# Optimization experiments

Hardware: AMD Instinct MI355X
Metric: run time of the kernel (lower is better)

The kernel has to match this reference:

```python
import jax, jax.numpy as jnp
import numpy as np

B, D, O = 1024, 512, 256


def setup_inputs() -> dict:
    key = jax.random.key(0)
    kx, kw, kt = jax.random.split(key, 3)
    x = jax.random.uniform(kx, (B, D), dtype=jnp.float32)
    w = jax.random.uniform(kw, (D, O), dtype=jnp.float32)
    t = jax.random.uniform(kt, (B, O), dtype=jnp.float32)
    return {"x": x, "w": w, "t": t}


def reference(x, w, t):
    xe = x[:, :, None]   # [B, D, 1]
    te = t[:, None, :]   # [B, 1, O]
    we = w[None, :, :]   # [1, D, O]

    x_comp = 1.0 - xe    # [B, D, 1]
    t_comp = 1.0 - te    # [B, 1, O]
    w_comp = 1.0 - we    # [1, D, O]

    # rel_x: [1, D, O]; sum over batch dim 0 of broadcasted min
    rel_x = 1.0 - (jnp.sum(jnp.minimum(x_comp, t_comp), axis=0, keepdims=True)
                   / jnp.sum(x_comp, axis=0, keepdims=True))
    # rel_w: [B, 1, O]; sum over D dim of broadcasted min
    rel_w = 1.0 - (jnp.sum(jnp.minimum(w_comp, t_comp), axis=-2, keepdims=True)
                   / jnp.sum(w_comp, axis=-2, keepdims=True))

    ind_x = jnp.argmin(jnp.maximum(xe, rel_x), axis=-2, keepdims=True)  # [B, 1, O]
    ind_w = jnp.argmin(jnp.maximum(rel_w, we), axis=-2, keepdims=True)  # [B, 1, O]

    inner_x = jnp.maximum(xe, jax.lax.stop_gradient(we))  # [B, D, O]
    inner_w = jnp.maximum(jax.lax.stop_gradient(xe), we)  # [B, D, O]

    chosen_x = jnp.take_along_axis(inner_x, ind_x, axis=-2).squeeze(-2)  # [B, O]
    chosen_w = jnp.take_along_axis(inner_w, ind_w, axis=-2).squeeze(-2)  # [B, O]
    return chosen_x, chosen_w
```

## Files before the change

### kernel.cpp

```cpp
#include <hip/hip_runtime.h>

#define BB 1024
#define DD 512
#define OO 256

__global__ __launch_bounds__(256) void kA(const float* __restrict__ x,
                                          const float* __restrict__ w,
                                          const float* __restrict__ t,
                                          float* __restrict__ xT,
                                          float* __restrict__ tT,
                                          float* __restrict__ wT,
                                          double* __restrict__ Sxp,
                                          double* __restrict__ part) {
  __shared__ float smem[32 * 33];
  int bid = blockIdx.x, tid = threadIdx.x;
  if (bid < 512) {
    float (*xl)[132] = (float(*)[132])smem;
    int dg = bid >> 3, sy = bid & 7;
    int d0 = dg * 8, b0 = sy * 128, o = tid;
    for (int i = tid; i < 1024; i += 256) {
      int bb = i >> 3, dd = i & 7;
      xl[dd][bb] = x[(b0 + bb) * DD + d0 + dd];
    }
    __syncthreads();
    double acc[8] = {0, 0, 0, 0, 0, 0, 0, 0};
    for (int bb = 0; bb < 128; bb += 2) {
      float tv0 = t[(b0 + bb) * OO + o];
      float tv1 = t[(b0 + bb + 1) * OO + o];
#pragma unroll
      for (int dd = 0; dd < 8; ++dd)
        acc[dd] += (double)fmaxf(xl[dd][bb], tv0) + (double)fmaxf(xl[dd][bb + 1], tv1);
    }
#pragma unroll
    for (int dd = 0; dd < 8; ++dd)
      part[(sy * DD + d0 + dd) * OO + o] = acc[dd];
  } else if (bid < 1024) {
    float (*tile)[33] = (float(*)[33])smem;
    int r = bid - 512;
    int b0 = (r & 31) * 32, d0 = (r >> 5) * 32;
    int tx = tid & 31, ty = tid >> 5;
    for (int i = 0; i < 32; i += 8)
      tile[ty + i][tx] = x[(b0 + ty + i) * DD + d0 + tx];
    __syncthreads();
    for (int i = 0; i < 32; i += 8)
      xT[(d0 + ty + i) * BB + b0 + tx] = tile[tx][ty + i];
  } else if (bid < 1280) {
    float (*tile)[33] = (float(*)[33])smem;
    int r = bid - 1024;
    int b0 = (r & 31) * 32, o0 = (r >> 5) * 32;
    int tx = tid & 31, ty = tid >> 5;
    for (int i = 0; i < 32; i += 8)
      tile[ty + i][tx] = t[(b0 + ty + i) * OO + o0 + tx];
    __syncthreads();
    for (int i = 0; i < 32; i += 8)
      tT[(o0 + ty + i) * BB + b0 + tx] = tile[tx][ty + i];
  } else if (bid < 1408) {
    float (*tile)[33] = (float(*)[33])smem;
    int r = bid - 1280;
    int d0 = (r & 15) * 32, o0 = (r >> 4) * 32;
    int tx = tid & 31, ty = tid >> 5;
    for (int i = 0; i < 32; i += 8)
      tile[ty + i][tx] = w[(d0 + ty + i) * OO + o0 + tx];
    __syncthreads();
    for (int i = 0; i < 32; i += 8)
      wT[(o0 + ty + i) * DD + d0 + tx] = tile[tx][ty + i];
  } else {
    int r = bid - 1408;
    int sy = r & 7, dh = r >> 3;
    int d = dh * 256 + tid, b0 = sy * 128;
    double s = 0.0;
    for (int b = b0; b < b0 + 128; ++b) s += 1.0 - (double)x[b * DD + d];
    Sxp[sy * DD + d] = s;
  }
}

__global__ __launch_bounds__(256) void kB(const float* __restrict__ wT,
                                          const double* __restrict__ Sxp,
                                          const double* __restrict__ part,
                                          float* __restrict__ sv_g,
                                          int* __restrict__ si_g,
                                          int* __restrict__ off_g,
                                          double* __restrict__ P_g,
                                          int* __restrict__ Mx_g,
                                          double* __restrict__ rv_g,
                                          int* __restrict__ ri_g,
                                          double* __restrict__ eb_g,
                                          double* __restrict__ hdrW,
                                          int* __restrict__ gmin_g) {
  int bid = blockIdx.x, tid = threadIdx.x;
  int lane = tid & 63, wid = tid >> 6;
  if (bid < OO) {
    int o = bid;
    __shared__ float sv[512];
    __shared__ int si[512];
    __shared__ int cnt[512];
    __shared__ int off[513];
    __shared__ double P[513];
    __shared__ int Mx[513];
    __shared__ double wsc[4];
    __shared__ int wmn[4];
    __shared__ unsigned long long wk[4];
    int i0 = 2 * tid, i1 = 2 * tid + 1;
    float w0 = wT[o * DD + i0], w1 = wT[o * DD + i1];
    cnt[i0] = 0; cnt[i1] = 0;
    __syncthreads();
    int q0 = min(511, max(0, (int)(w0 * 512.0f)));
    int q1 = min(511, max(0, (int)(w1 * 512.0f)));
    int sl0 = atomicAdd(&cnt[q0], 1);
    int sl1 = atomicAdd(&cnt[q1], 1);
    __syncthreads();
    {
      int e0 = cnt[i0], e1 = cnt[i1];
      int s = e0 + e1, v = s;
      for (int d = 1; d < 64; d <<= 1) {
        int u = __shfl_up(v, d);
        if (lane >= d) v += u;
      }
      if (lane == 63) wmn[wid] = v;
      __syncthreads();
      int wp = 0;
      for (int u = 0; u < wid; ++u) wp += wmn[u];
      int ex = wp + (v - s);
      off[i0] = ex; off[i1] = ex + e0;
      if (tid == 255) off[512] = ex + s;
      __syncthreads();
    }
    sv[off[q0] + sl0] = w0; si[off[q0] + sl0] = i0;
    sv[off[q1] + sl1] = w1; si[off[q1] + sl1] = i1;
    __syncthreads();
    for (int q = tid; q < 512; q += 256) {
      int s = off[q], e = off[q + 1];
      for (int i = s + 1; i < e; ++i) {
        int ki = si[i]; float kv = sv[i]; int j = i - 1;
        while (j >= s && si[j] > ki) { si[j + 1] = si[j]; sv[j + 1] = sv[j]; --j; }
        si[j + 1] = ki; sv[j + 1] = kv;
      }
    }
    __syncthreads();
    {
      double e0 = (double)sv[i0], e1 = (double)sv[i1];
      int m0 = si[i0], m1 = si[i1];
      double s = e0 + e1; int mm = min(m0, m1);
      double vs = s; int vm = mm;
      for (int d = 1; d < 64; d <<= 1) {
        double us = __shfl_up(vs, d);
        int um = __shfl_up(vm, d);
        if (lane >= d) { vs += us; vm = min(vm, um); }
      }
      double exs = __shfl_up(vs, 1);
      int exm = __shfl_up(vm, 1);
      if (lane == 0) { exs = 0.0; exm = 0x7fffffff; }
      if (lane == 63) { wsc[wid] = vs; wmn[wid] = vm; }
      __syncthreads();
      double wp = 0.0; int wm = 0x7fffffff;
      for (int u = 0; u < wid; ++u) { wp += wsc[u]; wm = min(wm, wmn[u]); }
      double EX = wp + exs; int EXM = min(wm, exm);
      P[i0] = EX; P[i1] = EX + e0;
      Mx[i0] = EXM; Mx[i1] = min(EXM, m0);
      if (tid == 255) { P[512] = EX + s; Mx[512] = min(EXM, mm); }
      __syncthreads();
    }
    {
      unsigned long long k0 = ((unsigned long long)__float_as_uint(sv[i0]) << 32) | (unsigned)si[i0];
      unsigned long long k1 = ((unsigned long long)__float_as_uint(sv[i1]) << 32) | (unsigned)si[i1];
      unsigned long long kk = k0 < k1 ? k0 : k1;
      for (int d = 32; d > 0; d >>= 1) {
        unsigned long long u = __shfl_down(kk, d);
        kk = u < kk ? u : kk;
      }
      if (lane == 0) wk[wid] = kk;
      __syncthreads();
      if (tid == 0) {
        unsigned long long g = wk[0];
        for (int u = 1; u < 4; ++u) g = wk[u] < g ? wk[u] : g;
        gmin_g[o] = (int)(g & 0xffffffffull);
      }
    }
    for (int i = tid; i < 512; i += 256) {
      sv_g[o * 512 + i] = sv[i];
      si_g[o * 512 + i] = si[i];
    }
    for (int i = tid; i < 513; i += 256) {
      off_g[o * 513 + i] = off[i];
      P_g[o * 513 + i] = P[i];
      Mx_g[o * 513 + i] = Mx[i];
    }
    if (tid == 0) { hdrW[o * 2 + 0] = 512.0 - P[512]; hdrW[o * 2 + 1] = P[512]; }
  } else {
    int o = bid - OO;
    __shared__ double rl[512];
    __shared__ int cnt2[512];
    __shared__ int roff[513];
    __shared__ double rv[512];
    __shared__ int ri[512];
    __shared__ double eb[512];
    __shared__ double wred[8];
    __shared__ int wint[4];
    int i0 = 2 * tid, i1 = 2 * tid + 1;
    {
      double sx0 = 0.0, sx1 = 0.0, a0 = 0.0, a1 = 0.0;
#pragma unroll
      for (int s = 0; s < 8; ++s) {
        sx0 += Sxp[s * DD + i0];
        sx1 += Sxp[s * DD + i1];
        a0 += part[(s * DD + i0) * OO + o];
        a1 += part[(s * DD + i1) * OO + o];
      }
      rl[i0] = 1.0 - (1024.0 - a0) / sx0;
      rl[i1] = 1.0 - (1024.0 - a1) / sx1;
    }
    double mn = fmin(rl[i0], rl[i1]), mx = fmax(rl[i0], rl[i1]);
    for (int d = 32; d > 0; d >>= 1) {
      mn = fmin(mn, __shfl_down(mn, d));
      mx = fmax(mx, __shfl_down(mx, d));
    }
    if (lane == 0) { wred[wid] = mn; wred[4 + wid] = mx; }
    cnt2[i0] = 0; cnt2[i1] = 0;
    __syncthreads();
    double rmin = fmin(fmin(wred[0], wred[1]), fmin(wred[2], wred[3]));
    double rmax = fmax(fmax(wred[4], wred[5]), fmax(wred[6], wred[7]));
    double range = rmax - rmin;
    double scale = (range > 0.0) ? (512.0 / range) : 0.0;
    double bw = range * (1.0 / 512.0);
    double base = rmin - range * 1e-9;
    int q0 = min(511, max(0, (int)((rl[i0] - rmin) * scale)));
    int q1 = min(511, max(0, (int)((rl[i1] - rmin) * scale)));
    int sl0 = atomicAdd(&cnt2[q0], 1);
    int sl1 = atomicAdd(&cnt2[q1], 1);
    __syncthreads();
    {
      int e0 = cnt2[i0], e1 = cnt2[i1];
      int s = e0 + e1, v = s;
      for (int d = 1; d < 64; d <<= 1) {
        int u = __shfl_up(v, d);
        if (lane >= d) v += u;
      }
      if (lane == 63) wint[wid] = v;
      __syncthreads();
      int wp = 0;
      for (int u = 0; u < wid; ++u) wp += wint[u];
      int ex = wp + (v - s);
      roff[i0] = ex; roff[i1] = ex + e0;
      if (tid == 255) roff[512] = ex + s;
      __syncthreads();
    }
    {
      int p0 = roff[q0] + sl0, p1 = roff[q1] + sl1;
      rv[p0] = rl[i0]; ri[p0] = i0; eb[p0] = base + (double)q0 * bw;
      rv[p1] = rl[i1]; ri[p1] = i1; eb[p1] = base + (double)q1 * bw;
    }
    __syncthreads();
    for (int i = tid; i < 512; i += 256) {
      rv_g[o * 512 + i] = rv[i];
      ri_g[o * 512 + i] = ri[i];
      eb_g[o * 512 + i] = eb[i];
    }
  }
}

__global__ __launch_bounds__(256) void kC(
    const float* __restrict__ xT, const float* __restrict__ wT,
    const float* __restrict__ tT, const float* __restrict__ sv_g,
    const int* __restrict__ si_g, const int* __restrict__ off_g,
    const double* __restrict__ P_g, const int* __restrict__ Mx_g,
    const double* __restrict__ rv_g, const int* __restrict__ ri_g,
    const double* __restrict__ eb_g, const double* __restrict__ hdrW,
    const int* __restrict__ gmin_g, float* __restrict__ out) {
  int o = blockIdx.x, tid = threadIdx.x;
  int b = blockIdx.y * 256 + tid;
  __shared__ float sv[512];
  __shared__ int si[512];
  __shared__ int off[513];
  __shared__ double P[513];
  __shared__ int Mx[513];
  __shared__ double rv[512];
  __shared__ int ri[512];
  __shared__ double eb[512];
  for (int i = tid; i < 512; i += 256) {
    sv[i] = sv_g[o * 512 + i];
    si[i] = si_g[o * 512 + i];
    rv[i] = rv_g[o * 512 + i];
    ri[i] = ri_g[o * 512 + i];
    eb[i] = eb_g[o * 512 + i];
  }
  for (int i = tid; i < 513; i += 256) {
    off[i] = off_g[o * 513 + i];
    P[i] = P_g[o * 513 + i];
    Mx[i] = Mx_g[o * 513 + i];
  }
  __syncthreads();
  double Sw = hdrW[o * 2 + 0], Wtot = hdrW[o * 2 + 1];
  float c = tT[o * BB + b];
  int j = min(511, max(0, (int)(c * 512.0f)));
  int s0 = off[j], e0 = off[j + 1];
  double pre = P[s0];
  int k = s0;
  for (int i = s0; i < e0; ++i) {
    float wv = sv[i];
    if (wv <= c) { pre += (double)wv; ++k; }
  }
  double smax = (Wtot - pre) + (double)c * (double)k;
  double relw = 1.0 - (512.0 - smax) / Sw;
  int j2t = (int)(relw * 512.0);
  int j2 = min(511, max(0, j2t));
  int s2 = off[j2], e2 = off[j2 + 1];
  int iw = Mx[s2];
  for (int i = s2; i < e2; ++i)
    if ((double)sv[i] <= relw) iw = min(iw, si[i]);
  if (iw == 0x7fffffff) iw = gmin_g[o];
  float x0 = xT[ri[0] * BB + b], x1 = xT[ri[1] * BB + b];
  float x2 = xT[ri[2] * BB + b], x3 = xT[ri[3] * BB + b];
  float x4 = xT[ri[4] * BB + b], x5 = xT[ri[5] * BB + b];
  float x6 = xT[ri[6] * BB + b], x7 = xT[ri[7] * BB + b];
  double best = 1e300;
  int bix = 0x7fffffff;
  for (int i = 0; i < 512; ++i) {
    if (eb[i] > best) break;
    int dj = ri[i];
    float xv;
    if (i < 8) {
      xv = (i == 0) ? x0 : (i == 1) ? x1 : (i == 2) ? x2 : (i == 3) ? x3
         : (i == 4) ? x4 : (i == 5) ? x5 : (i == 6) ? x6 : x7;
    } else {
      xv = xT[dj * BB + b];
    }
    double v = fmax((double)xv, rv[i]);
    if (v < best || (v == best && dj < bix)) { best = v; bix = dj; }
  }
  float ox = fmaxf(xT[bix * BB + b], wT[o * DD + bix]);
  float ow = fmaxf(xT[iw * BB + b], wT[o * DD + iw]);
  out[b * OO + o] = ox;
  out[BB * OO + b * OO + o] = ow;
}

extern "C" void kernel_launch(void* const* d_in, const int* in_sizes, int n_in,
                              void* d_out, int out_size, void* d_ws,
                              size_t ws_size, hipStream_t stream) {
  const float* x = (const float*)d_in[0];
  const float* w = (const float*)d_in[1];
  const float* t = (const float*)d_in[2];
  float* out = (float*)d_out;
  char* ws = (char*)d_ws;

  size_t off = 0;
  float* xT    = (float*)(ws + off);  off += (size_t)DD * BB * 4;
  float* tT    = (float*)(ws + off);  off += (size_t)OO * BB * 4;
  float* wT    = (float*)(ws + off);  off += (size_t)OO * DD * 4;
  double* Sxp  = (double*)(ws + off); off += (size_t)8 * DD * 8;
  double* part = (double*)(ws + off); off += (size_t)8 * DD * OO * 8;
  float* sv_g  = (float*)(ws + off);  off += (size_t)OO * 512 * 4;
  int* si_g    = (int*)(ws + off);    off += (size_t)OO * 512 * 4;
  int* off_g   = (int*)(ws + off);    off += (size_t)OO * 513 * 4;
  double* P_g  = (double*)(ws + off); off += (size_t)OO * 513 * 8;
  int* Mx_g    = (int*)(ws + off);    off += (size_t)OO * 513 * 4;
  double* rv_g = (double*)(ws + off); off += (size_t)OO * 512 * 8;
  int* ri_g    = (int*)(ws + off);    off += (size_t)OO * 512 * 4;
  double* eb_g = (double*)(ws + off); off += (size_t)OO * 512 * 8;
  double* hdrW = (double*)(ws + off); off += (size_t)OO * 2 * 8;
  int* gmin_g  = (int*)(ws + off);    off += (size_t)OO * 4;

  kA<<<1424, 256, 0, stream>>>(x, w, t, xT, tT, wT, Sxp, part);
  kB<<<2 * OO, 256, 0, stream>>>(wT, Sxp, part, sv_g, si_g, off_g, P_g, Mx_g,
                                 rv_g, ri_g, eb_g, hdrW, gmin_g);
  kC<<<dim3(OO, BB / 256), 256, 0, stream>>>(xT, wT, tT, sv_g, si_g, off_g,
                                             P_g, Mx_g, rv_g, ri_g, eb_g,
                                             hdrW, gmin_g, out);
}
```

Before: 67.95 us.

## Vectorize x loads in kA, shrink bucket bounds to float, cache w row in LDS

kA now loads x with float4 global reads and reads the LDS tile as float4 while processing four batch rows per iteration. The bucket lower bounds eb are stored as float, rounded down, which halves their workspace and shared-memory footprint. kC copies the w row into shared memory and keeps the winning x value from the argmin loop, which removes two scattered global gathers at the end. The relw bucket scan now spans two buckets, likely to cover rounding near bucket edges, at the cost of a little more scanning.

```diff
diff --git a/kernel.cpp b/kernel.cpp
--- a/kernel.cpp
+++ b/kernel.cpp
@@ -12,24 +12,34 @@
                                           float* __restrict__ wT,
                                           double* __restrict__ Sxp,
                                           double* __restrict__ part) {
-  __shared__ float smem[32 * 33];
+  __shared__ float smem[8 * 136];
   int bid = blockIdx.x, tid = threadIdx.x;
   if (bid < 512) {
-    float (*xl)[132] = (float(*)[132])smem;
+    float (*xl)[136] = (float(*)[136])smem;
     int dg = bid >> 3, sy = bid & 7;
     int d0 = dg * 8, b0 = sy * 128, o = tid;
-    for (int i = tid; i < 1024; i += 256) {
-      int bb = i >> 3, dd = i & 7;
-      xl[dd][bb] = x[(b0 + bb) * DD + d0 + dd];
+    {
+      int bb = tid >> 1, half = tid & 1;
+      float4 g = *(const float4*)&x[(b0 + bb) * DD + d0 + half * 4];
+      xl[half * 4 + 0][bb] = g.x;
+      xl[half * 4 + 1][bb] = g.y;
+      xl[half * 4 + 2][bb] = g.z;
+      xl[half * 4 + 3][bb] = g.w;
     }
     __syncthreads();
     double acc[8] = {0, 0, 0, 0, 0, 0, 0, 0};
-    for (int bb = 0; bb < 128; bb += 2) {
-      float tv0 = t[(b0 + bb) * OO + o];
+    for (int bb = 0; bb < 128; bb += 4) {
+      float tv0 = t[(b0 + bb + 0) * OO + o];
       float tv1 = t[(b0 + bb + 1) * OO + o];
+      float tv2 = t[(b0 + bb + 2) * OO + o];
+      float tv3 = t[(b0 + bb + 3) * OO + o];
 #pragma unroll
-      for (int dd = 0; dd < 8; ++dd)
-        acc[dd] += (double)fmaxf(xl[dd][bb], tv0) + (double)fmaxf(xl[dd][bb + 1], tv1);
+      for (int dd = 0; dd < 8; ++dd) {
+        float4 xv = *(const float4*)&xl[dd][bb];
+        double s01 = (double)fmaxf(xv.x, tv0) + (double)fmaxf(xv.y, tv1);
+        double s23 = (double)fmaxf(xv.z, tv2) + (double)fmaxf(xv.w, tv3);
+        acc[dd] += s01 + s23;
+      }
     }
 #pragma unroll
     for (int dd = 0; dd < 8; ++dd)
@@ -84,7 +94,7 @@
                                           int* __restrict__ Mx_g,
                                           double* __restrict__ rv_g,
                                           int* __restrict__ ri_g,
-                                          double* __restrict__ eb_g,
+                                          float* __restrict__ eb_g,
                                           double* __restrict__ hdrW,
                                           int* __restrict__ gmin_g) {
   int bid = blockIdx.x, tid = threadIdx.x;
@@ -193,7 +203,7 @@
     __shared__ int roff[513];
     __shared__ double rv[512];
     __shared__ int ri[512];
-    __shared__ double eb[512];
+    __shared__ float eb[512];
     __shared__ double wred[8];
     __shared__ int wint[4];
     int i0 = 2 * tid, i1 = 2 * tid + 1;
@@ -246,8 +256,10 @@
     }
     {
       int p0 = roff[q0] + sl0, p1 = roff[q1] + sl1;
-      rv[p0] = rl[i0]; ri[p0] = i0; eb[p0] = base + (double)q0 * bw;
-      rv[p1] = rl[i1]; ri[p1] = i1; eb[p1] = base + (double)q1 * bw;
+      rv[p0] = rl[i0]; ri[p0] = i0;
+      eb[p0] = __double2float_rd(base + (double)q0 * bw);
+      rv[p1] = rl[i1]; ri[p1] = i1;
+      eb[p1] = __double2float_rd(base + (double)q1 * bw);
     }
     __syncthreads();
     for (int i = tid; i < 512; i += 256) {
@@ -264,7 +276,7 @@
     const int* __restrict__ si_g, const int* __restrict__ off_g,
     const double* __restrict__ P_g, const int* __restrict__ Mx_g,
     const double* __restrict__ rv_g, const int* __restrict__ ri_g,
-    const double* __restrict__ eb_g, const double* __restrict__ hdrW,
+    const float* __restrict__ eb_g, const double* __restrict__ hdrW,
     const int* __restrict__ gmin_g, float* __restrict__ out) {
   int o = blockIdx.x, tid = threadIdx.x;
   int b = blockIdx.y * 256 + tid;
@@ -275,13 +287,15 @@
   __shared__ int Mx[513];
   __shared__ double rv[512];
   __shared__ int ri[512];
-  __shared__ double eb[512];
+  __shared__ float eb[512];
+  __shared__ float wl[512];
   for (int i = tid; i < 512; i += 256) {
     sv[i] = sv_g[o * 512 + i];
     si[i] = si_g[o * 512 + i];
     rv[i] = rv_g[o * 512 + i];
     ri[i] = ri_g[o * 512 + i];
     eb[i] = eb_g[o * 512 + i];
+    wl[i] = wT[o * DD + i];
   }
   for (int i = tid; i < 513; i += 256) {
     off[i] = off_g[o * 513 + i];
@@ -301,9 +315,8 @@
   }
   double smax = (Wtot - pre) + (double)c * (double)k;
   double relw = 1.0 - (512.0 - smax) / Sw;
-  int j2t = (int)(relw * 512.0);
-  int j2 = min(511, max(0, j2t));
-  int s2 = off[j2], e2 = off[j2 + 1];
+  int j2 = min(511, max(0, (int)(relw * 512.0)));
+  int s2 = off[j2], e2 = off[min(512, j2 + 2)];
   int iw = Mx[s2];
   for (int i = s2; i < e2; ++i)
     if ((double)sv[i] <= relw) iw = min(iw, si[i]);
@@ -314,8 +327,9 @@
   float x6 = xT[ri[6] * BB + b], x7 = xT[ri[7] * BB + b];
   double best = 1e300;
   int bix = 0x7fffffff;
+  float bestx = 0.0f;
   for (int i = 0; i < 512; ++i) {
-    if (eb[i] > best) break;
+    if ((double)eb[i] > best) break;
     int dj = ri[i];
     float xv;
     if (i < 8) {
@@ -325,10 +339,10 @@
       xv = xT[dj * BB + b];
     }
     double v = fmax((double)xv, rv[i]);
-    if (v < best || (v == best && dj < bix)) { best = v; bix = dj; }
-  }
-  float ox = fmaxf(xT[bix * BB + b], wT[o * DD + bix]);
-  float ow = fmaxf(xT[iw * BB + b], wT[o * DD + iw]);
+    if (v < best || (v == best && dj < bix)) { best = v; bix = dj; bestx = xv; }
+  }
+  float ox = fmaxf(bestx, wl[bix]);
+  float ow = fmaxf(xT[iw * BB + b], wl[iw]);
   out[b * OO + o] = ox;
   out[BB * OO + b * OO + o] = ow;
 }
@@ -355,7 +369,7 @@
   int* Mx_g    = (int*)(ws + off);    off += (size_t)OO * 513 * 4;
   double* rv_g = (double*)(ws + off); off += (size_t)OO * 512 * 8;
   int* ri_g    = (int*)(ws + off);    off += (size_t)OO * 512 * 4;
-  double* eb_g = (double*)(ws + off); off += (size_t)OO * 512 * 8;
+  float* eb_g  = (float*)(ws + off);  off += (size_t)OO * 512 * 4;
   double* hdrW = (double*)(ws + off); off += (size_t)OO * 2 * 8;
   int* gmin_g  = (int*)(ws + off);    off += (size_t)OO * 4;
 
```

Result: faster. 63.98 us (-5.8%).
